# Performance work log

Measured on AMD Instinct MI355X. Metric: run time of the kernel, lower is better.

## Reference

```python
import jax, jax.numpy as jnp
import numpy as np

BETA = 0.9
T = 16
THR = 1.0
SLOPE = 25.0  # snntorch surrogate.fast_sigmoid default slope


@jax.custom_vjp
def spike(x):
    # Heaviside forward, fast-sigmoid surrogate backward (snntorch fast_sigmoid)
    return (x > 0.0).astype(x.dtype)

def _spike_fwd(x):
    return spike(x), x

def _spike_bwd(x, g):
    return (g / (SLOPE * jnp.abs(x) + 1.0) ** 2,)

spike.defvjp(_spike_fwd, _spike_bwd)


def conv1d(x, w, b, pad):
    # x: (B, C_in, L), w: (C_out, C_in, K)
    y = jax.lax.conv_general_dilated(
        x, w, window_strides=(1,), padding=[(pad, pad)],
        dimension_numbers=("NCH", "OIH", "NCH"))
    return y + b[None, :, None]


def lif(cur, mem):
    # snntorch Leaky, reset_mechanism='subtract', threshold=1.0.
    # reset spike is computed from the PREVIOUS membrane and detached.
    reset = jax.lax.stop_gradient((mem > THR).astype(cur.dtype))
    mem = BETA * mem + cur - reset * THR
    spk = spike(mem - THR)
    return spk, mem


def setup_inputs() -> dict:
    key = jax.random.key(0)
    ks = jax.random.split(key, 14)

    def u(k, shape, fan_in):
        bound = 1.0 / np.sqrt(fan_in)
        return jax.random.uniform(k, shape, jnp.float32, -bound, bound)

    x = jax.random.normal(ks[0], (2048, 2, 128), dtype=jnp.float32)
    W1 = u(ks[1], (256, 2, 5), 2 * 5);    b1 = u(ks[2], (256,), 2 * 5)
    W2 = u(ks[3], (128, 256, 3), 256 * 3); b2 = u(ks[4], (128,), 256 * 3)
    W3 = u(ks[5], (64, 128, 3), 128 * 3);  b3 = u(ks[6], (64,), 128 * 3)
    W4 = u(ks[7], (2, 64, 3), 64 * 3);     b4 = u(ks[8], (2,), 64 * 3)
    fw1 = u(ks[9], (100, 256), 256);       fb1 = u(ks[10], (100,), 256)
    fw2 = u(ks[11], (40, 100), 100);       fb2 = u(ks[12], (40,), 100)
    return {"x": x, "W1": W1, "b1": b1, "W2": W2, "b2": b2,
            "W3": W3, "b3": b3, "W4": W4, "b4": b4,
            "fw1": fw1, "fb1": fb1, "fw2": fw2, "fb2": fb2}


def reference(x, W1, b1, W2, b2, W3, b3, W4, b4, fw1, fb1, fw2, fb2):
    B, _, L = x.shape
    f32 = x.dtype
    # conv1 input is constant across timesteps -> hoist (same math)
    cur1 = conv1d(x, W1, b1, 2)
    init = (jnp.zeros((B, 256, L), f32), jnp.zeros((B, 128, L), f32),
            jnp.zeros((B, 64, L), f32), jnp.zeros((B, 2, L), f32),
            jnp.zeros((B, 100), f32), jnp.zeros((B, 40), f32))

    def step(carry, _):
        m1, m2, m3, m4, m5, acc = carry
        s1, m1 = lif(cur1, m1)
        s2, m2 = lif(conv1d(s1, W2, b2, 1), m2)
        s3, m3 = lif(conv1d(s2, W3, b3, 1), m3)
        s4, m4 = lif(conv1d(s3, W4, b4, 1), m4)
        flat = s4.reshape(B, -1)                      # (B, 256)
        s5, m5 = lif(flat @ fw1.T + fb1, m5)
        acc = acc + s5 @ fw2.T + fb2
        return (m1, m2, m3, m4, m5, acc), None

    (_, _, _, _, _, acc), _ = jax.lax.scan(step, init, None, length=T)
    return acc / T
```

## Files before the change

kernel.cpp:

```cpp
#include <hip/hip_runtime.h>
#include <stdint.h>

#define BETA 0.9f

typedef unsigned short u16;
typedef unsigned char u8;
typedef _Float16 f16x8 __attribute__((ext_vector_type(8)));
typedef float f32x4 __attribute__((ext_vector_type(4)));

__device__ __forceinline__ void async_copy16(const void* g, void* l) {
  __builtin_amdgcn_global_load_lds(
      (const __attribute__((address_space(1))) uint32_t*)g,
      (__attribute__((address_space(3))) uint32_t*)l, 16, 0, 0);
}

__device__ __forceinline__ uint4 expandB4(uint32_t byte) {
  uint32_t z = byte | (byte << 15);
  uint4 r;
  r.x = ((z >> 0) & 0x10001u) << 12;
  r.y = ((z >> 2) & 0x10001u) << 12;
  r.z = ((z >> 4) & 0x10001u) << 12;
  r.w = ((z >> 6) & 0x10001u) << 12;
  return r;
}

__global__ void prep_kernel(const float* __restrict__ W2, const float* __restrict__ W3,
                            const float* __restrict__ fw1, const float* __restrict__ fw2,
                            u16* __restrict__ A2c, u16* __restrict__ A3c,
                            float* __restrict__ fw1T, float* __restrict__ fw2T) {
  int o = blockIdx.x * 256 + threadIdx.x;
  if (o < 98304) {
    int tap = o >> 15, r = o & 32767, co = r >> 8, ci = r & 255;
    float w = W2[(co * 256 + ci) * 3 + tap];
    float h = (float)(_Float16)w;
    _Float16 hv = (_Float16)(h * 2048.0f);
    _Float16 mv = (_Float16)((w - h) * 2048.0f);
    u16 hb, mb;
    __builtin_memcpy(&hb, &hv, 2);
    __builtin_memcpy(&mb, &mv, 2);
    int c = ci >> 5, cl = ci & 31;
    int ct = co >> 6, col = co & 63;
    int g = ((cl >> 3) ^ ((co >> 1) & 3)) & 3;
    int pos = g * 8 + (cl & 7);
    A2c[((((c * 2 + 0) * 2 + ct) * 3 + tap) * 64 + col) * 32 + pos] = hb;
    A2c[((((c * 2 + 1) * 2 + ct) * 3 + tap) * 64 + col) * 32 + pos] = mb;
  }
  int o2 = o - 98304;
  if (o2 >= 0 && o2 < 24576) {
    int tap = o2 >> 13, r = o2 & 8191, co = r >> 7, ci = r & 127;
    float w = W3[(co * 128 + ci) * 3 + tap];
    float h = (float)(_Float16)w;
    _Float16 hv = (_Float16)(h * 2048.0f);
    _Float16 mv = (_Float16)((w - h) * 2048.0f);
    u16 hb, mb;
    __builtin_memcpy(&hb, &hv, 2);
    __builtin_memcpy(&mb, &mv, 2);
    int c = ci >> 5, cl = ci & 31;
    int g = ((cl >> 3) ^ ((co >> 1) & 3)) & 3;
    int pos = g * 8 + (cl & 7);
    A3c[(((c * 2 + 0) * 3 + tap) * 64 + co) * 32 + pos] = hb;
    A3c[(((c * 2 + 1) * 3 + tap) * 64 + co) * 32 + pos] = mb;
  }
  int o3 = o - (98304 + 24576);
  if (o3 >= 0 && o3 < 25600) {
    int f = o3 / 100, i = o3 % 100;
    fw1T[o3] = fw1[i * 256 + f];
  }
  int o4 = o - (98304 + 24576 + 25600);
  if (o4 >= 0 && o4 < 4000) {
    int i = o4 / 40, j = o4 % 40;
    fw2T[o4] = fw2[j * 100 + i];
  }
}

__global__ __launch_bounds__(256) void conv1_lif_kernel(
    const float* __restrict__ x, const float* __restrict__ W1,
    const float* __restrict__ b1, u8* __restrict__ SBT2) {
  __shared__ float xl[2][132];
  __shared__ u16 bl[8][128];
  int b = blockIdx.x, g = blockIdx.y;
  int tid = threadIdx.x;
  for (int i = tid; i < 264; i += 256) {
    int ci = i / 132, idx = i % 132, lg = idx - 2;
    xl[ci][idx] = (lg >= 0 && lg < 128) ? x[(b * 2 + ci) * 128 + lg] : 0.0f;
  }
  __syncthreads();
  int cosub = tid >> 5, tx = tid & 31;
  int co = g * 8 + cosub;
  float w[2][5];
#pragma unroll
  for (int ci = 0; ci < 2; ++ci)
#pragma unroll
    for (int k = 0; k < 5; ++k) w[ci][k] = W1[(co * 2 + ci) * 5 + k];
  float bias = b1[co];
  float cur[4];
#pragma unroll
  for (int j = 0; j < 4; ++j) {
    float acc = bias;
#pragma unroll
    for (int ci = 0; ci < 2; ++ci)
#pragma unroll
      for (int k = 0; k < 5; ++k) acc += w[ci][k] * xl[ci][4 * tx + j + k];
    cur[j] = acc;
  }
  float m[4] = {0.f, 0.f, 0.f, 0.f}, sp[4] = {0.f, 0.f, 0.f, 0.f};
  uint32_t bits[4] = {0u, 0u, 0u, 0u};
#pragma unroll
  for (int t = 0; t < 16; ++t) {
#pragma unroll
    for (int j = 0; j < 4; ++j) {
      m[j] = BETA * m[j] + cur[j] - sp[j];
      bool s = m[j] > 1.0f;
      bits[j] |= ((uint32_t)s) << t;
      sp[j] = s ? 1.0f : 0.0f;
    }
  }
#pragma unroll
  for (int j = 0; j < 4; ++j) bl[cosub][4 * tx + j] = (u16)bits[j];
  __syncthreads();
  if (tid < 128) {
    int l = tid;
    uint32_t wv[8];
#pragma unroll
    for (int j = 0; j < 8; ++j) wv[j] = bl[j][l];
    uint32_t ov[4];
#pragma unroll
    for (int k = 0; k < 4; ++k) {
      uint32_t v = 0;
#pragma unroll
      for (int tt = 0; tt < 4; ++tt) {
        int t = k * 4 + tt;
        uint32_t by = 0;
#pragma unroll
        for (int j = 0; j < 8; ++j) by |= ((wv[j] >> t) & 1u) << j;
        v |= by << (8 * tt);
      }
      ov[k] = v;
    }
    *(uint4*)(SBT2 + ((size_t)(b * 128 + l) * 32 + g) * 16) =
        make_uint4(ov[0], ov[1], ov[2], ov[3]);
  }
}

template <int CIN, int COUT, bool SBTOUT>
__global__ __launch_bounds__(256, 3) void conv_mfma_kernel(
    const u8* __restrict__ SBT, const u16* __restrict__ Agc,
    const float* __restrict__ bias, void* __restrict__ outp) {
  constexpr int NPHYS = CIN / 32;
  constexpr int NVIRT = 2 * NPHYS;
  constexpr int NCT = COUT / 64;
  constexpr int MT = 2;
  constexpr int NT = 8;
  constexpr int GB = CIN / 8;
  constexpr int ABYTES = 3 * 64 * 32 * 2;
  constexpr int AW = ABYTES / 4;
  constexpr int AISS = AW / 1024;
  constexpr int BSTR = 40;
  __shared__ __align__(16) char lds[2 * ABYTES];
  __shared__ __align__(16) u16 Bs[18 * 16 * BSTR];

  int b = blockIdx.x, lb = blockIdx.y * 16, ct = blockIdx.z;
  int tid = threadIdx.x, lane = tid & 63, wid = tid >> 6;
  int wx = wid & 1, wy = wid >> 1;
  int q = lane >> 4, xx = lane & 15;
  int mloc = wy * 32;
  int qs8 = (q ^ ((xx >> 1) & 3)) * 8;

  f32x4 acc[MT][NT];
#pragma unroll
  for (int mt = 0; mt < MT; ++mt)
#pragma unroll
    for (int nt = 0; nt < NT; ++nt) acc[mt][nt] = (f32x4){0.f, 0.f, 0.f, 0.f};

  auto stage_load = [&](int pn, int s) -> uint32_t {
    int row = s >> 4, g = (s >> 2) & 3, tq = s & 3;
    int l_in = lb + row - 1;
    if ((unsigned)l_in >= 128u) return 0u;
    return *(const uint32_t*)(SBT + ((size_t)(b * 128 + l_in) * GB + pn * 4 + g) * 16 + tq * 4);
  };
  auto stage_write = [&](int s, uint32_t w4) {
    int row = s >> 4, g = (s >> 2) & 3, tq = s & 3;
#pragma unroll
    for (int i = 0; i < 4; ++i) {
      uint32_t by = (w4 >> (8 * i)) & 0xFFu;
      int t = tq * 4 + i;
      *(uint4*)(Bs + (row * 16 + t) * BSTR + g * 8) = expandB4(by);
    }
  };

  uint32_t w4a = stage_load(0, tid);
  uint32_t w4b = (tid < 32) ? stage_load(0, tid + 256) : 0u;
  {
    const char* gsrc = (const char*)Agc + (size_t)ct * ABYTES +
                       (size_t)wid * AW + lane * 16;
    char* ldst = lds + wid * AW;
#pragma unroll
    for (int i = 0; i < AISS; ++i) async_copy16(gsrc + i * 1024, ldst + i * 1024);
  }

  f16x8 Bf[10];
#pragma unroll 2
  for (int v = 0; v < NVIRT; ++v) {
    __syncthreads();
    if ((v & 1) == 0) {
      stage_write(tid, w4a);
      if (tid < 32) stage_write(tid + 256, w4b);
      __syncthreads();
    }
    if (v + 1 < NVIRT) {
      const char* gsrc = (const char*)Agc + ((size_t)(v + 1) * NCT + ct) * ABYTES +
                         (size_t)wid * AW + lane * 16;
      char* ldst = lds + ((v + 1) & 1) * ABYTES + wid * AW;
#pragma unroll
      for (int i = 0; i < AISS; ++i) async_copy16(gsrc + i * 1024, ldst + i * 1024);
    }
    if ((v & 1) == 0) {
      int pn = (v >> 1) + 1;
      if (pn < NPHYS) {
        w4a = stage_load(pn, tid);
        if (tid < 32) w4b = stage_load(pn, tid + 256);
      }
#pragma unroll
      for (int u = 0; u < 10; ++u)
        Bf[u] = *(const f16x8*)(Bs + ((wx * 8 + u) * 16 + xx) * BSTR + q * 8);
    }
    const u16* Asv = (const u16*)(lds + (v & 1) * ABYTES);
#pragma unroll
    for (int tap = 0; tap < 3; ++tap)
#pragma unroll
      for (int mt = 0; mt < MT; ++mt) {
        f16x8 Af = *(const f16x8*)(Asv + ((size_t)(tap * 64 + mloc + mt * 16 + xx)) * 32 + qs8);
#pragma unroll
        for (int nt = 0; nt < NT; ++nt)
          acc[mt][nt] = __builtin_amdgcn_mfma_f32_16x16x32_f16(
              Af, Bf[nt + tap], acc[mt][nt], 0, 0, 0);
      }
  }
  __syncthreads();

  float* scr = (float*)(void*)lds + wid * 1216;
  u16* bl = (u16*)(lds + 19456);
#pragma unroll
  for (int mt = 0; mt < MT; ++mt) {
#pragma unroll
    for (int h = 0; h < 2; ++h) {
#pragma unroll
      for (int u2 = 0; u2 < 4; ++u2)
#pragma unroll
        for (int r = 0; r < 4; ++r)
          scr[(u2 * 16 + q * 4 + r) * 19 + xx] = acc[mt][h * 4 + u2][r];
      __syncthreads();
      int col = mloc + mt * 16 + xx;
      float bc = bias[ct * 64 + col];
      const float* rowp = scr + (q * 16 + xx) * 19;
      float mm = 0.f, sp = 0.f;
      uint32_t bits = 0;
#pragma unroll
      for (int t = 0; t < 16; ++t) {
        float cur = rowp[t] + bc;
        mm = BETA * mm + cur - sp;
        bool s = mm > 1.0f;
        bits |= ((uint32_t)s) << t;
        sp = s ? 1.0f : 0.0f;
      }
      bl[col * 16 + wx * 8 + h * 4 + q] = (u16)bits;
      __syncthreads();
    }
  }

  if constexpr (SBTOUT) {
    constexpr int GBo = COUT / 8;
    if (tid < 128) {
      int g = tid & 7, ll = tid >> 3;
      uint32_t wv[8];
#pragma unroll
      for (int j = 0; j < 8; ++j) wv[j] = bl[(8 * g + j) * 16 + ll];
      uint32_t ov[4];
#pragma unroll
      for (int k = 0; k < 4; ++k) {
        uint32_t v = 0;
#pragma unroll
        for (int tt = 0; tt < 4; ++tt) {
          int t = k * 4 + tt;
          uint32_t by = 0;
#pragma unroll
          for (int j = 0; j < 8; ++j) by |= ((wv[j] >> t) & 1u) << j;
          v |= by << (8 * tt);
        }
        ov[k] = v;
      }
      *(uint4*)((u8*)outp + ((size_t)(b * 128 + lb + ll) * GBo + ct * 8 + g) * 16) =
          make_uint4(ov[0], ov[1], ov[2], ov[3]);
    }
  } else {
    if (tid < 128) {
      int col = tid >> 1, hf = tid & 1;
      uint4 v = *(const uint4*)(bl + col * 16 + hf * 8);
      *(uint4*)((u16*)outp + ((size_t)b * COUT + ct * 64 + col) * 128 + lb + hf * 8) = v;
    }
  }
}

__global__ __launch_bounds__(256) void head_kernel(
    const u16* __restrict__ s3bits, const float* __restrict__ W4,
    const float* __restrict__ b4, const float* __restrict__ fw1T,
    const float* __restrict__ fb1, const float* __restrict__ fw2T,
    const float* __restrict__ fb2, float* __restrict__ out) {
  __shared__ u16 s3l[64][130];
  __shared__ float W4l[384];
  __shared__ u16 flat4[256];
  __shared__ u16 s5b[100];
  int b = blockIdx.x, tid = threadIdx.x;

  for (int i = tid; i < 64 * 130; i += 256) {
    int ci = i / 130, idx = i % 130, lg = idx - 1;
    s3l[ci][idx] = (lg >= 0 && lg < 128) ? s3bits[((size_t)b * 64 + ci) * 128 + lg] : (u16)0;
  }
  for (int i = tid; i < 384; i += 256) W4l[i] = W4[i];
  __syncthreads();

  {
    int co = tid >> 7, l = tid & 127;
    float acc4[16];
#pragma unroll
    for (int t = 0; t < 16; ++t) acc4[t] = 0.f;
    for (int ci = 0; ci < 64; ++ci) {
#pragma unroll
      for (int k = 0; k < 3; ++k) {
        float wv = W4l[(co * 64 + ci) * 3 + k];
        uint32_t msk = s3l[ci][l + k];
#pragma unroll
        for (int t = 0; t < 16; ++t)
          acc4[t] = fmaf(wv, (float)((msk >> t) & 1u), acc4[t]);
      }
    }
    float bc = b4[co];
    float m = 0.f, sp = 0.f;
    uint32_t bits = 0;
#pragma unroll
    for (int t = 0; t < 16; ++t) {
      m = BETA * m + (acc4[t] + bc) - sp;
      bool s = m > 1.0f;
      bits |= ((uint32_t)s) << t;
      sp = s ? 1.0f : 0.0f;
    }
    flat4[tid] = (u16)bits;
  }
  __syncthreads();

  if (tid < 100) {
    float acc5[16];
#pragma unroll
    for (int t = 0; t < 16; ++t) acc5[t] = 0.f;
    for (int f = 0; f < 256; ++f) {
      float wv = fw1T[f * 100 + tid];
      uint32_t msk = flat4[f];
#pragma unroll
      for (int t = 0; t < 16; ++t)
        acc5[t] = fmaf(wv, (float)((msk >> t) & 1u), acc5[t]);
    }
    float bc = fb1[tid];
    float m = 0.f, sp = 0.f;
    uint32_t bits = 0;
#pragma unroll
    for (int t = 0; t < 16; ++t) {
      m = BETA * m + (acc5[t] + bc) - sp;
      bool s = m > 1.0f;
      bits |= ((uint32_t)s) << t;
      sp = s ? 1.0f : 0.0f;
    }
    s5b[tid] = (u16)bits;
  }
  __syncthreads();

  if (tid < 40) {
    float a = 0.f;
    for (int i = 0; i < 100; ++i) {
      float wv = fw2T[i * 40 + tid];
      a = fmaf(wv, (float)__popc((uint32_t)s5b[i]), a);
    }
    out[b * 40 + tid] = a * 0.0625f + fb2[tid];
  }
}

extern "C" void kernel_launch(void* const* d_in, const int* in_sizes, int n_in,
                              void* d_out, int out_size, void* d_ws, size_t ws_size,
                              hipStream_t stream) {
  const float* x   = (const float*)d_in[0];
  const float* W1  = (const float*)d_in[1];
  const float* b1  = (const float*)d_in[2];
  const float* W2  = (const float*)d_in[3];
  const float* b2  = (const float*)d_in[4];
  const float* W3  = (const float*)d_in[5];
  const float* b3  = (const float*)d_in[6];
  const float* W4  = (const float*)d_in[7];
  const float* b4  = (const float*)d_in[8];
  const float* fw1 = (const float*)d_in[9];
  const float* fb1 = (const float*)d_in[10];
  const float* fw2 = (const float*)d_in[11];
  const float* fb2 = (const float*)d_in[12];
  float* out = (float*)d_out;

  char* ws = (char*)d_ws;
  u16*   A2c  = (u16*)(ws);
  u16*   A3c  = (u16*)(ws + 393216);
  float* fw1T = (float*)(ws + 491520);
  float* fw2T = (float*)(ws + 593920);
  u8*    SBT2 = (u8*)(ws + 610304);
  u8*    SBT3 = (u8*)(ws + 610304 + 134217728);
  u16*   s3b  = (u16*)(ws + 610304 + 134217728 + 67108864);

  prep_kernel<<<dim3(596), dim3(256), 0, stream>>>(W2, W3, fw1, fw2, A2c, A3c, fw1T, fw2T);
  conv1_lif_kernel<<<dim3(2048, 32), dim3(256), 0, stream>>>(x, W1, b1, SBT2);
  conv_mfma_kernel<256, 128, true><<<dim3(2048, 8, 2), dim3(256), 0, stream>>>(SBT2, A2c, b2, SBT3);
  conv_mfma_kernel<128, 64, false><<<dim3(2048, 8, 1), dim3(256), 0, stream>>>(SBT3, A3c, b3, s3b);
  head_kernel<<<dim3(2048), dim3(256), 0, stream>>>(s3b, W4, b4, fw1T, fb1, fw2T, fb2, out);
}
```

Measured before the change: 2.044 ms.

## Replace split-fp16 conv MFMA with three-plane int8 MFMA on binary spikes

Weights for conv2/conv3 are now decomposed into three signed int8 digit planes (scales 2^11, 2^18, 2^25) instead of an fp16 hi/lo pair, and the conv uses the i32 16x16x64 int8 MFMA on 0/1 spike inputs. Partial sums are accumulated in int32, with the accumulator shifted left by 7 between planes (Horner style), then scaled back to float. The intent is to double K per MFMA, halve operand bytes for weights and spikes in LDS, and keep near-fp32 accuracy through integer-exact accumulation. The cost is 3 passes instead of 2 per channel chunk, a B-stage rewrite every pass, and a risk of int8 digit overflow or int32 overflow.

```diff
diff --git a/kernel.cpp b/kernel.cpp
--- a/kernel.cpp
+++ b/kernel.cpp
@@ -5,8 +5,8 @@
 
 typedef unsigned short u16;
 typedef unsigned char u8;
-typedef _Float16 f16x8 __attribute__((ext_vector_type(8)));
-typedef float f32x4 __attribute__((ext_vector_type(4)));
+typedef signed char i8;
+typedef int i32x4 __attribute__((ext_vector_type(4)));
 
 __device__ __forceinline__ void async_copy16(const void* g, void* l) {
   __builtin_amdgcn_global_load_lds(
@@ -14,52 +14,46 @@
       (__attribute__((address_space(3))) uint32_t*)l, 16, 0, 0);
 }
 
-__device__ __forceinline__ uint4 expandB4(uint32_t byte) {
-  uint32_t z = byte | (byte << 15);
-  uint4 r;
-  r.x = ((z >> 0) & 0x10001u) << 12;
-  r.y = ((z >> 2) & 0x10001u) << 12;
-  r.z = ((z >> 4) & 0x10001u) << 12;
-  r.w = ((z >> 6) & 0x10001u) << 12;
-  return r;
-}
-
 __global__ void prep_kernel(const float* __restrict__ W2, const float* __restrict__ W3,
                             const float* __restrict__ fw1, const float* __restrict__ fw2,
-                            u16* __restrict__ A2c, u16* __restrict__ A3c,
+                            i8* __restrict__ A2c, i8* __restrict__ A3c,
                             float* __restrict__ fw1T, float* __restrict__ fw2T) {
   int o = blockIdx.x * 256 + threadIdx.x;
   if (o < 98304) {
     int tap = o >> 15, r = o & 32767, co = r >> 8, ci = r & 255;
     float w = W2[(co * 256 + ci) * 3 + tap];
-    float h = (float)(_Float16)w;
-    _Float16 hv = (_Float16)(h * 2048.0f);
-    _Float16 mv = (_Float16)((w - h) * 2048.0f);
-    u16 hb, mb;
-    __builtin_memcpy(&hb, &hv, 2);
-    __builtin_memcpy(&mb, &mv, 2);
-    int c = ci >> 5, cl = ci & 31;
+    float d0 = __builtin_rintf(w * 0x1p11f);
+    float r1 = w - d0 * 0x1p-11f;
+    float d1 = __builtin_rintf(r1 * 0x1p18f);
+    float r2 = r1 - d1 * 0x1p-18f;
+    float d2 = __builtin_rintf(r2 * 0x1p25f);
+    int cp = ci >> 6, cl = ci & 63;
     int ct = co >> 6, col = co & 63;
-    int g = ((cl >> 3) ^ ((co >> 1) & 3)) & 3;
-    int pos = g * 8 + (cl & 7);
-    A2c[((((c * 2 + 0) * 2 + ct) * 3 + tap) * 64 + col) * 32 + pos] = hb;
-    A2c[((((c * 2 + 1) * 2 + ct) * 3 + tap) * 64 + col) * 32 + pos] = mb;
+    int gs = ((cl >> 4) ^ ((col >> 1) & 3)) & 3;
+    int pos = gs * 16 + (cl & 15);
+    size_t base = ((size_t)((0 * 4 + cp) * 2 + ct) * 3 + tap) * 64 * 64 + col * 64 + pos;
+    size_t pstride = (size_t)4 * 2 * 3 * 64 * 64;
+    A2c[base] = (i8)(int)d0;
+    A2c[pstride + base] = (i8)(int)d1;
+    A2c[2 * pstride + base] = (i8)(int)d2;
   }
   int o2 = o - 98304;
   if (o2 >= 0 && o2 < 24576) {
     int tap = o2 >> 13, r = o2 & 8191, co = r >> 7, ci = r & 127;
     float w = W3[(co * 128 + ci) * 3 + tap];
-    float h = (float)(_Float16)w;
-    _Float16 hv = (_Float16)(h * 2048.0f);
-    _Float16 mv = (_Float16)((w - h) * 2048.0f);
-    u16 hb, mb;
-    __builtin_memcpy(&hb, &hv, 2);
-    __builtin_memcpy(&mb, &mv, 2);
-    int c = ci >> 5, cl = ci & 31;
-    int g = ((cl >> 3) ^ ((co >> 1) & 3)) & 3;
-    int pos = g * 8 + (cl & 7);
-    A3c[(((c * 2 + 0) * 3 + tap) * 64 + co) * 32 + pos] = hb;
-    A3c[(((c * 2 + 1) * 3 + tap) * 64 + co) * 32 + pos] = mb;
+    float d0 = __builtin_rintf(w * 0x1p11f);
+    float r1 = w - d0 * 0x1p-11f;
+    float d1 = __builtin_rintf(r1 * 0x1p18f);
+    float r2 = r1 - d1 * 0x1p-18f;
+    float d2 = __builtin_rintf(r2 * 0x1p25f);
+    int cp = ci >> 6, cl = ci & 63;
+    int gs = ((cl >> 4) ^ ((co >> 1) & 3)) & 3;
+    int pos = gs * 16 + (cl & 15);
+    size_t base = ((size_t)(0 * 2 + cp) * 3 + tap) * 64 * 64 + co * 64 + pos;
+    size_t pstride = (size_t)2 * 3 * 64 * 64;
+    A3c[base] = (i8)(int)d0;
+    A3c[pstride + base] = (i8)(int)d1;
+    A3c[2 * pstride + base] = (i8)(int)d2;
   }
   int o3 = o - (98304 + 24576);
   if (o3 >= 0 && o3 < 25600) {
@@ -144,52 +138,54 @@
 
 template <int CIN, int COUT, bool SBTOUT>
 __global__ __launch_bounds__(256, 3) void conv_mfma_kernel(
-    const u8* __restrict__ SBT, const u16* __restrict__ Agc,
+    const u8* __restrict__ SBT, const i8* __restrict__ Agc,
     const float* __restrict__ bias, void* __restrict__ outp) {
-  constexpr int NPHYS = CIN / 32;
-  constexpr int NVIRT = 2 * NPHYS;
+  constexpr int NCP = CIN / 64;
+  constexpr int NVIRT = 3 * NCP;
   constexpr int NCT = COUT / 64;
   constexpr int MT = 2;
   constexpr int NT = 8;
   constexpr int GB = CIN / 8;
-  constexpr int ABYTES = 3 * 64 * 32 * 2;
+  constexpr int ABYTES = 3 * 64 * 64;
   constexpr int AW = ABYTES / 4;
   constexpr int AISS = AW / 1024;
-  constexpr int BSTR = 40;
   __shared__ __align__(16) char lds[2 * ABYTES];
-  __shared__ __align__(16) u16 Bs[18 * 16 * BSTR];
+  __shared__ __align__(16) u8 Bs[18 * 16 * 80];
 
   int b = blockIdx.x, lb = blockIdx.y * 16, ct = blockIdx.z;
   int tid = threadIdx.x, lane = tid & 63, wid = tid >> 6;
   int wx = wid & 1, wy = wid >> 1;
   int q = lane >> 4, xx = lane & 15;
   int mloc = wy * 32;
-  int qs8 = (q ^ ((xx >> 1) & 3)) * 8;
-
-  f32x4 acc[MT][NT];
+  int gs16 = ((q ^ ((xx >> 1) & 3)) & 3) * 16;
+
+  i32x4 acc[MT][NT];
 #pragma unroll
   for (int mt = 0; mt < MT; ++mt)
 #pragma unroll
-    for (int nt = 0; nt < NT; ++nt) acc[mt][nt] = (f32x4){0.f, 0.f, 0.f, 0.f};
-
-  auto stage_load = [&](int pn, int s) -> uint32_t {
-    int row = s >> 4, g = (s >> 2) & 3, tq = s & 3;
+    for (int nt = 0; nt < NT; ++nt) acc[mt][nt] = (i32x4){0, 0, 0, 0};
+
+  auto stage_load = [&](int cp, int s) -> uint32_t {
+    int row = s >> 5, gl = s & 7, tq = (s >> 3) & 3;
     int l_in = lb + row - 1;
     if ((unsigned)l_in >= 128u) return 0u;
-    return *(const uint32_t*)(SBT + ((size_t)(b * 128 + l_in) * GB + pn * 4 + g) * 16 + tq * 4);
+    return *(const uint32_t*)(SBT + ((size_t)(b * 128 + l_in) * GB + cp * 8 + gl) * 16 + tq * 4);
   };
   auto stage_write = [&](int s, uint32_t w4) {
-    int row = s >> 4, g = (s >> 2) & 3, tq = s & 3;
+    int row = s >> 5, gl = s & 7, tq = (s >> 3) & 3;
 #pragma unroll
     for (int i = 0; i < 4; ++i) {
       uint32_t by = (w4 >> (8 * i)) & 0xFFu;
+      uint32_t lo = ((by & 0xFu) * 0x204081u) & 0x01010101u;
+      uint32_t hi = ((by >> 4) * 0x204081u) & 0x01010101u;
       int t = tq * 4 + i;
-      *(uint4*)(Bs + (row * 16 + t) * BSTR + g * 8) = expandB4(by);
+      *(uint2*)(Bs + (row * 16 + t) * 80 + gl * 8) = make_uint2(lo, hi);
     }
   };
 
   uint32_t w4a = stage_load(0, tid);
-  uint32_t w4b = (tid < 32) ? stage_load(0, tid + 256) : 0u;
+  uint32_t w4b = stage_load(0, tid + 256);
+  uint32_t w4c = (tid < 64) ? stage_load(0, tid + 512) : 0u;
   {
     const char* gsrc = (const char*)Agc + (size_t)ct * ABYTES +
                        (size_t)wid * AW + lane * 16;
@@ -198,41 +194,42 @@
     for (int i = 0; i < AISS; ++i) async_copy16(gsrc + i * 1024, ldst + i * 1024);
   }
 
-  f16x8 Bf[10];
-#pragma unroll 2
   for (int v = 0; v < NVIRT; ++v) {
     __syncthreads();
-    if ((v & 1) == 0) {
-      stage_write(tid, w4a);
-      if (tid < 32) stage_write(tid + 256, w4b);
-      __syncthreads();
-    }
+    stage_write(tid, w4a);
+    stage_write(tid + 256, w4b);
+    if (tid < 64) stage_write(tid + 512, w4c);
+    __syncthreads();
     if (v + 1 < NVIRT) {
       const char* gsrc = (const char*)Agc + ((size_t)(v + 1) * NCT + ct) * ABYTES +
                          (size_t)wid * AW + lane * 16;
       char* ldst = lds + ((v + 1) & 1) * ABYTES + wid * AW;
 #pragma unroll
       for (int i = 0; i < AISS; ++i) async_copy16(gsrc + i * 1024, ldst + i * 1024);
-    }
-    if ((v & 1) == 0) {
-      int pn = (v >> 1) + 1;
-      if (pn < NPHYS) {
-        w4a = stage_load(pn, tid);
-        if (tid < 32) w4b = stage_load(pn, tid + 256);
-      }
-#pragma unroll
-      for (int u = 0; u < 10; ++u)
-        Bf[u] = *(const f16x8*)(Bs + ((wx * 8 + u) * 16 + xx) * BSTR + q * 8);
-    }
-    const u16* Asv = (const u16*)(lds + (v & 1) * ABYTES);
+      int cpn = (v + 1) % NCP;
+      w4a = stage_load(cpn, tid);
+      w4b = stage_load(cpn, tid + 256);
+      if (tid < 64) w4c = stage_load(cpn, tid + 512);
+    }
+    if (v > 0 && (v % NCP) == 0) {
+#pragma unroll
+      for (int mt = 0; mt < MT; ++mt)
+#pragma unroll
+        for (int nt = 0; nt < NT; ++nt) acc[mt][nt] = acc[mt][nt] << 7;
+    }
+    i32x4 Bf[10];
+#pragma unroll
+    for (int u = 0; u < 10; ++u)
+      Bf[u] = *(const i32x4*)(Bs + ((wx * 8 + u) * 16 + xx) * 80 + q * 16);
+    const i8* Asv = (const i8*)(lds + (v & 1) * ABYTES);
 #pragma unroll
     for (int tap = 0; tap < 3; ++tap)
 #pragma unroll
       for (int mt = 0; mt < MT; ++mt) {
-        f16x8 Af = *(const f16x8*)(Asv + ((size_t)(tap * 64 + mloc + mt * 16 + xx)) * 32 + qs8);
+        i32x4 Af = *(const i32x4*)(Asv + (tap * 64 + mloc + mt * 16 + xx) * 64 + gs16);
 #pragma unroll
         for (int nt = 0; nt < NT; ++nt)
-          acc[mt][nt] = __builtin_amdgcn_mfma_f32_16x16x32_f16(
+          acc[mt][nt] = __builtin_amdgcn_mfma_i32_16x16x64_i8(
               Af, Bf[nt + tap], acc[mt][nt], 0, 0, 0);
       }
   }
@@ -248,7 +245,8 @@
       for (int u2 = 0; u2 < 4; ++u2)
 #pragma unroll
         for (int r = 0; r < 4; ++r)
-          scr[(u2 * 16 + q * 4 + r) * 19 + xx] = acc[mt][h * 4 + u2][r];
+          scr[(u2 * 16 + q * 4 + r) * 19 + xx] =
+              (float)acc[mt][h * 4 + u2][r] * 0x1p-25f;
       __syncthreads();
       int col = mloc + mt * 16 + xx;
       float bc = bias[ct * 64 + col];
@@ -402,13 +400,13 @@
   float* out = (float*)d_out;
 
   char* ws = (char*)d_ws;
-  u16*   A2c  = (u16*)(ws);
-  u16*   A3c  = (u16*)(ws + 393216);
-  float* fw1T = (float*)(ws + 491520);
-  float* fw2T = (float*)(ws + 593920);
-  u8*    SBT2 = (u8*)(ws + 610304);
-  u8*    SBT3 = (u8*)(ws + 610304 + 134217728);
-  u16*   s3b  = (u16*)(ws + 610304 + 134217728 + 67108864);
+  i8*    A2c  = (i8*)(ws);
+  i8*    A3c  = (i8*)(ws + 294912);
+  float* fw1T = (float*)(ws + 368640);
+  float* fw2T = (float*)(ws + 471040);
+  u8*    SBT2 = (u8*)(ws + 487424);
+  u8*    SBT3 = (u8*)(ws + 487424 + 134217728);
+  u16*   s3b  = (u16*)(ws + 487424 + 134217728 + 67108864);
 
   prep_kernel<<<dim3(596), dim3(256), 0, stream>>>(W2, W3, fw1, fw2, A2c, A3c, fw1T, fw2T);
   conv1_lif_kernel<<<dim3(2048, 32), dim3(256), 0, stream>>>(x, W1, b1, SBT2);
```

New measurement: 1.948 ms. 4.7% less time.
